# Optimization experiments

Measured on AMD Instinct MI355X. Metric: run time of the kernel, lower is better.

## Reference

```python
import jax, jax.numpy as jnp
import numpy as np
import math

B_SZ, T, D_IN, D_OUT, N = 8, 4096, 1024, 1024, 512
RMIN, RMAX, MAX_PHASE = 0.9, 1.0, 6.283


def setup_inputs() -> dict:
    key = jax.random.key(0)
    ks = jax.random.split(key, 9)
    x = jax.random.normal(ks[0], (B_SZ, T, D_IN), dtype=jnp.float32)
    u1 = jax.random.uniform(ks[1], (N,), dtype=jnp.float32)
    u2 = jax.random.uniform(ks[2], (N,), dtype=jnp.float32)
    nu_log = jnp.log(-0.5 * jnp.log(u1 * (RMAX + RMIN) * (RMAX - RMIN) + RMIN ** 2))
    theta_log = jnp.log(MAX_PHASE * u2)
    lam_mod = jnp.exp(-jnp.exp(nu_log))
    gamma_log = jnp.log(jnp.sqrt(1.0 - jnp.square(lam_mod)))
    B_re = jax.random.normal(ks[3], (N, D_IN), dtype=jnp.float32) / math.sqrt(2 * D_IN)
    B_im = jax.random.normal(ks[4], (N, D_IN), dtype=jnp.float32) / math.sqrt(2 * D_IN)
    C_re = jax.random.normal(ks[5], (D_OUT, N), dtype=jnp.float32) / math.sqrt(N)
    C_im = jax.random.normal(ks[6], (D_OUT, N), dtype=jnp.float32) / math.sqrt(N)
    D = jax.random.normal(ks[7], (D_OUT, D_IN), dtype=jnp.float32) / math.sqrt(D_IN)
    return {"x": x, "nu_log": nu_log, "theta_log": theta_log, "gamma_log": gamma_log,
            "B_re": B_re, "B_im": B_im, "C_re": C_re, "C_im": C_im, "D": D}


def reference(x, nu_log, theta_log, gamma_log, B_re, B_im, C_re, C_im, D):
    # Diagonal complex transition Lambda = exp(-exp(nu_log)) * exp(i*exp(theta_log))
    lam = jnp.exp(-jnp.exp(nu_log) + 1j * jnp.exp(theta_log))  # [N] complex64
    gamma = jnp.exp(gamma_log)  # [N]
    Bmat = B_re + 1j * B_im  # [N, D_IN]
    # Input projection for all timesteps at once: b_t = gamma * (B @ u_t)
    Bu = jnp.einsum('bti,ni->btn', x.astype(Bmat.dtype), Bmat) * gamma  # [B,T,N] complex
    # Parallel (associative) scan of x_t = lam * x_{t-1} + b_t over the time axis
    A = jnp.broadcast_to(lam, Bu.shape)

    def combine(e1, e2):
        a1, b1 = e1
        a2, b2 = e2
        return a1 * a2, a2 * b1 + b2

    _, states = jax.lax.associative_scan(combine, (A, Bu), axis=1)  # states: [B,T,N] complex
    Cmat = C_re + 1j * C_im  # [D_OUT, N]
    y = jnp.einsum('btn,on->bto', states, Cmat).real + jnp.einsum('bti,oi->bto', x, D)
    return y
```

## Files before the change

kernel.cpp:

```cpp
#include <hip/hip_runtime.h>
#include <stdint.h>


#define BSZ   8
#define TLEN  4096
#define DIN   1024
#define DOUT  1024
#define NST   512
#define M_TOT (BSZ * TLEN)
#define NC    32
#define CL    128

#define WOFF  8192
#define NBUF  16384

#define PLA   4096
#define OBUFS 12288

typedef __attribute__((ext_vector_type(8))) short bf16x8;
typedef __attribute__((ext_vector_type(4))) float f32x4;

__device__ __forceinline__ float s2f(short s) {
  unsigned v = ((unsigned)(unsigned short)s) << 16;
  return __builtin_bit_cast(float, v);
}
__device__ __forceinline__ short f2s_rne(float f) {
  unsigned u = __builtin_bit_cast(unsigned, f);
  unsigned r = (u + 0x7FFFu + ((u >> 16) & 1u)) >> 16;
  return (short)r;
}
__device__ __forceinline__ void round8(const float4 v0, const float4 v1, bf16x8& hv) {
  const float f[8] = {v0.x, v0.y, v0.z, v0.w, v1.x, v1.y, v1.z, v1.w};
  #pragma unroll
  for (int j = 0; j < 8; ++j) hv[j] = f2s_rne(f[j]);
}

__device__ __forceinline__ void gload16(const short* g, short* l) {
  __builtin_amdgcn_global_load_lds(
      (const __attribute__((address_space(1))) void*)g,
      (__attribute__((address_space(3))) void*)l, 16, 0, 0);
}


__device__ __forceinline__ void stage256(
    const short* __restrict__ Ag, const short* __restrict__ Wg,
    const int lda, const int ldb, const int m0, const int n0, const int k0,
    short* lbuf, const int w, const int lane)
{
  const int q  = (lane & 3) ^ ((lane >> 3) & 3);
  const int gr = lane >> 2;
  #pragma unroll
  for (int j = 0; j < 4; ++j) {
    const int ch = w * 4 + j;
    const short* g;
    int r0, ld, dst;
    if (ch < 16) { g = Ag; r0 = m0 + ch * 16;        ld = lda; dst = ch * 512; }
    else         { g = Wg; r0 = n0 + (ch - 16) * 16; ld = ldb; dst = WOFF + (ch - 16) * 512; }
    gload16(g + (size_t)(r0 + gr) * ld + k0 + q * 8, lbuf + dst);
  }
}

template<int NT>
__device__ __forceinline__ void gemm256(
    const short* __restrict__ Ap, const short* __restrict__ Wp,
    const int lda, const int ldb, const int m0, const int n0, const int tid,
    f32x4 (&acc)[8][4], short* lds)
{
  const int lane = tid & 63, w = tid >> 6, wm = w >> 2, wn = w & 3;
  const int lr = lane & 15, kg = lane >> 4;
  const int qo = (kg ^ ((lr >> 1) & 3)) * 8;

  stage256(Ap, Wp, lda, ldb, m0, n0, 0, lds, w, lane);

  for (int k = 0; k < NT; ++k) {
    short* cur = lds + (k & 1) * NBUF;
    if (k + 1 < NT) {
      stage256(Ap, Wp, lda, ldb, m0, n0, (k + 1) * 32,
               lds + ((k + 1) & 1) * NBUF, w, lane);
      asm volatile("s_waitcnt vmcnt(4)" ::: "memory");
    } else {
      asm volatile("s_waitcnt vmcnt(0)" ::: "memory");
    }
    __builtin_amdgcn_s_barrier();

    bf16x8 wv[4];
    #pragma unroll
    for (int ph = 0; ph < 2; ++ph) {
      if (ph == 0) {
        #pragma unroll
        for (int nf = 0; nf < 4; ++nf)
          wv[nf] = *(const bf16x8*)&cur[WOFF + (wn * 64 + nf * 16 + lr) * 32 + qo];
      }
      bf16x8 af[4];
      #pragma unroll
      for (int mi = 0; mi < 4; ++mi)
        af[mi] = *(const bf16x8*)&cur[(wm * 128 + (ph * 4 + mi) * 16 + lr) * 32 + qo];
      __builtin_amdgcn_s_barrier();
      asm volatile("s_waitcnt lgkmcnt(0)" ::: "memory");
      __builtin_amdgcn_sched_barrier(0);
      __builtin_amdgcn_s_setprio(1);
      #pragma unroll
      for (int nf = 0; nf < 4; ++nf)
        #pragma unroll
        for (int mi = 0; mi < 4; ++mi)
          acc[ph * 4 + mi][nf] =
              __builtin_amdgcn_mfma_f32_16x16x32_bf16(af[mi], wv[nf], acc[ph * 4 + mi][nf], 0, 0, 0);
      __builtin_amdgcn_s_setprio(0);
      __builtin_amdgcn_s_barrier();
    }
  }
}

__device__ __forceinline__ void map256(const int bid, int& mb, int& nb) {
  const int xcd = bid & 7;
  const int j   = bid >> 3;
  mb = xcd * 16 + (j >> 2);
  nb = j & 3;
}

__device__ __forceinline__ void stage_cx(
    const short* __restrict__ Ag, const short* __restrict__ Wg,
    const int lda, const int ldb, const int m0, const int n0, const int k0,
    short* lbuf, const int w, const int lane)
{
  const int q  = (lane & 3) ^ ((lane >> 3) & 3);
  const int gr = lane >> 2;
  #pragma unroll
  for (int j = 0; j < 3; ++j) {
    const int ch = w * 3 + j;
    const short* g;
    int r0, ld, dst;
    if (ch < 8) { g = Ag; r0 = m0 + ch * 16;        ld = lda; dst = ch * 512; }
    else        { g = Wg; r0 = n0 + (ch - 8) * 16;  ld = ldb; dst = PLA + (ch - 8) * 512; }
    gload16(g + (size_t)(r0 + gr) * ld + k0 + q * 8, lbuf + dst);
  }
}

__device__ __forceinline__ void gemm_fb(
    const float* __restrict__ Af, const short* __restrict__ Wp,
    const int lda, const int ldb, const int K, const int m0, const int n0, const int tid,
    f32x4 (&acc)[4][4], short* lds)
{
  const int lane = tid & 63, w = tid >> 6, wm = w >> 2, wn = w & 3;
  const int r = tid & 127, e = (tid >> 7) & 3;
  float4 pa[2];
  {
    const float* p = Af + (size_t)(m0 + r) * lda + e * 8;
    pa[0] = *(const float4*)(p);
    pa[1] = *(const float4*)(p + 4);
  }
  for (int k0 = 0; k0 < K; k0 += 32) {
    __syncthreads();
    {
      bf16x8 hv;
      round8(pa[0], pa[1], hv);
      const int f = (r >> 1) & 3;
      *(bf16x8*)&lds[r * 32 + ((e ^ f) * 8)] = hv;
    }
    {
      const int q = (lane & 3) ^ ((lane >> 3) & 3);
      const int gr = lane >> 2;
      #pragma unroll
      for (int i = 0; i < 2; ++i)
        gload16(Wp + (size_t)(n0 + (2 * w + i) * 16 + gr) * ldb + k0 + q * 8,
                lds + PLA + (2 * w + i) * 512);
    }
    __syncthreads();
    if (k0 + 32 < K) {
      const float* p = Af + (size_t)(m0 + r) * lda + (k0 + 32) + e * 8;
      pa[0] = *(const float4*)(p);
      pa[1] = *(const float4*)(p + 4);
    }
    const int lr = lane & 15, kg = lane >> 4;
    const int qo = (kg ^ ((lr >> 1) & 3)) * 8;
    bf16x8 aw[4], bw[4];
    #pragma unroll
    for (int mi = 0; mi < 4; ++mi)
      aw[mi] = *(const bf16x8*)&lds[(wm * 64 + mi * 16 + lr) * 32 + qo];
    #pragma unroll
    for (int ni = 0; ni < 4; ++ni)
      bw[ni] = *(const bf16x8*)&lds[PLA + (wn * 64 + ni * 16 + lr) * 32 + qo];
    #pragma unroll
    for (int ni = 0; ni < 4; ++ni)
      #pragma unroll
      for (int mi = 0; mi < 4; ++mi)
        acc[mi][ni] = __builtin_amdgcn_mfma_f32_16x16x32_bf16(aw[mi], bw[ni], acc[mi][ni], 0, 0, 0);
  }
  __syncthreads();
}

template<int NT>
__device__ __forceinline__ void gemm_pl(
    const short* __restrict__ Ap, const short* __restrict__ Wp,
    const int lda, const int ldb, const int m0, const int n0, const int tid,
    f32x4 (&acc)[4][4], short* lds)
{
  const int lane = tid & 63, w = tid >> 6, wm = w >> 2, wn = w & 3;
  const int lr = lane & 15, kg = lane >> 4;
  const int qo = (kg ^ ((lr >> 1) & 3)) * 8;
  stage_cx(Ap, Wp, lda, ldb, m0, n0, 0, lds, w, lane);
  for (int k = 0; k < NT; ++k) {
    short* cur = lds + (k & 1) * OBUFS;
    if (k + 1 < NT) {
      stage_cx(Ap, Wp, lda, ldb, m0, n0, (k + 1) * 32, lds + ((k + 1) & 1) * OBUFS, w, lane);
      asm volatile("s_waitcnt vmcnt(3)" ::: "memory");
    } else {
      asm volatile("s_waitcnt vmcnt(0)" ::: "memory");
    }
    __builtin_amdgcn_s_barrier();
    bf16x8 bw[4];
    #pragma unroll
    for (int ph = 0; ph < 2; ++ph) {
      if (ph == 0) {
        #pragma unroll
        for (int ni = 0; ni < 4; ++ni)
          bw[ni] = *(const bf16x8*)&cur[PLA + (wn * 64 + ni * 16 + lr) * 32 + qo];
      }
      const int mi0 = ph * 2;
      const bf16x8 a0 = *(const bf16x8*)&cur[(wm * 64 + mi0 * 16 + lr) * 32 + qo];
      const bf16x8 a1 = *(const bf16x8*)&cur[(wm * 64 + (mi0 + 1) * 16 + lr) * 32 + qo];
      __builtin_amdgcn_s_barrier();
      asm volatile("s_waitcnt lgkmcnt(0)" ::: "memory");
      __builtin_amdgcn_sched_barrier(0);
      __builtin_amdgcn_s_setprio(1);
      #pragma unroll
      for (int ni = 0; ni < 4; ++ni) {
        acc[mi0][ni]     = __builtin_amdgcn_mfma_f32_16x16x32_bf16(a0, bw[ni], acc[mi0][ni], 0, 0, 0);
        acc[mi0 + 1][ni] = __builtin_amdgcn_mfma_f32_16x16x32_bf16(a1, bw[ni], acc[mi0 + 1][ni], 0, 0, 0);
      }
      __builtin_amdgcn_s_setprio(0);
      __builtin_amdgcn_s_barrier();
    }
  }
}

__device__ __forceinline__ void map_mn4(const int bid, int& mb, int& nb) {
  const int xcd = bid & 7;
  const int j   = bid >> 3;
  mb = xcd * 32 + (j >> 2);
  nb = j & 3;
}

__global__ __launch_bounds__(256) void wround_k(const float* __restrict__ src,
    short* __restrict__ h, const int n4, const float sgn)
{
  const int i = blockIdx.x * 256 + threadIdx.x;
  if (i >= n4) return;
  const float4 v = ((const float4*)src)[i];
  short4 hv;
  hv.x = f2s_rne(sgn * v.x); hv.y = f2s_rne(sgn * v.y);
  hv.z = f2s_rne(sgn * v.z); hv.w = f2s_rne(sgn * v.w);
  ((short4*)h)[i] = hv;
}

__global__ __launch_bounds__(512, 2) void bu_mfma(
    const short* __restrict__ xw,
    const short* __restrict__ Brw, const short* __restrict__ Biw,
    const float* __restrict__ gamma,
    short* __restrict__ bu_re, short* __restrict__ bu_im)
{
  __shared__ short lds[2 * NBUF];
  f32x4 acc[8][4] = {};
  const int tid = threadIdx.x;
  int mb, nbk;
  map256(blockIdx.x, mb, nbk);
  const int m0  = mb * 256;
  const int n0s = nbk * 256;
  const bool re = (n0s < NST);
  const int nb0 = n0s & (NST - 1);

  gemm256<32>(xw, re ? Brw : Biw, DIN, DIN, m0, nb0, tid, acc, lds);

  short* Hp = re ? bu_re : bu_im;
  const int lane = tid & 63, w = tid >> 6, wm = w >> 2, wn = w & 3;
  const int lr = lane & 15, lq = lane >> 4;
  #pragma unroll
  for (int nf = 0; nf < 4; ++nf) {
    const int nb = nb0 + wn * 64 + nf * 16 + lr;
    const float g = gamma[nb];
    #pragma unroll
    for (int mf = 0; mf < 8; ++mf)
      #pragma unroll
      for (int j = 0; j < 4; ++j) {
        const size_t m = (size_t)m0 + wm * 128 + mf * 16 + lq * 4 + j;
        Hp[m * NST + nb] = f2s_rne(acc[mf][nf][j] * g);
      }
  }
}

__global__ __launch_bounds__(512, 4) void bu_fb(
    const float* __restrict__ x,
    const short* __restrict__ Brw, const short* __restrict__ Biw,
    const float* __restrict__ gamma,
    short* __restrict__ bu_re, short* __restrict__ bu_im)
{
  __shared__ short lds[2 * OBUFS];
  f32x4 acc[4][4] = {};
  const int tid = threadIdx.x;
  int mb, nbk;
  map_mn4(blockIdx.x, mb, nbk);
  const int m0  = mb * 128;
  const int n0s = nbk * 256;
  const bool re = (n0s < NST);
  const int nb0 = n0s & (NST - 1);
  gemm_fb(x, re ? Brw : Biw, DIN, DIN, DIN, m0, nb0, tid, acc, lds);
  short* Hp = re ? bu_re : bu_im;
  const int lane = tid & 63, w = tid >> 6, wm = w >> 2, wn = w & 3;
  const int lr = lane & 15, lq = lane >> 4;
  #pragma unroll
  for (int ni = 0; ni < 4; ++ni) {
    const int nb = nb0 + wn * 64 + ni * 16 + lr;
    const float g = gamma[nb];
    #pragma unroll
    for (int mi = 0; mi < 4; ++mi)
      #pragma unroll
      for (int j = 0; j < 4; ++j) {
        const size_t m = (size_t)m0 + wm * 64 + mi * 16 + lq * 4 + j;
        Hp[m * NST + nb] = f2s_rne(acc[mi][ni][j] * g);
      }
  }
}

__global__ void params_k(const float* __restrict__ nulog, const float* __restrict__ thlog,
                         const float* __restrict__ glog,
                         float2* __restrict__ lam, float2* __restrict__ lamL,
                         float* __restrict__ gamma)
{
  const int n = blockIdx.x * 256 + threadIdx.x;
  if (n >= NST) return;
  const float nu = expf(nulog[n]);
  const float th = expf(thlog[n]);
  const float mod = expf(-nu);
  float s, c;
  sincosf(th, &s, &c);
  lam[n] = make_float2(mod * c, mod * s);
  const float modL = expf(-(float)CL * nu);
  float sL, cL;
  sincosf((float)CL * th, &sL, &cL);
  lamL[n] = make_float2(modL * cL, modL * sL);
  gamma[n] = expf(glog[n]);
}

__global__ __launch_bounds__(256) void scan_partial(
    const short* __restrict__ bu_re, const short* __restrict__ bu_im,
    const float2* __restrict__ lam, float2* __restrict__ carry)
{
  const int g = blockIdx.x * 256 + threadIdx.x;
  const int n2 = g & 255;
  const int c  = (g >> 8) & (NC - 1);
  const int b  = g >> 13;
  const int n  = n2 * 2;
  const float2 L0 = lam[n], L1 = lam[n + 1];
  const short2* R = (const short2*)bu_re;
  const short2* I = (const short2*)bu_im;
  size_t idx = ((size_t)b * TLEN + (size_t)c * CL) * (NST / 2) + n2;
  float sr0 = 0.f, si0 = 0.f, sr1 = 0.f, si1 = 0.f;
  #pragma unroll 4
  for (int t = 0; t < CL; ++t, idx += NST / 2) {
    const short2 vr = R[idx], vi = I[idx];
    const float br0 = s2f(vr.x), br1 = s2f(vr.y);
    const float bi0 = s2f(vi.x), bi1 = s2f(vi.y);
    float nr = fmaf(L0.x, sr0, fmaf(-L0.y, si0, br0));
    float ni = fmaf(L0.x, si0, fmaf( L0.y, sr0, bi0));
    sr0 = nr; si0 = ni;
    nr = fmaf(L1.x, sr1, fmaf(-L1.y, si1, br1));
    ni = fmaf(L1.x, si1, fmaf( L1.y, sr1, bi1));
    sr1 = nr; si1 = ni;
  }
  const size_t cb = (size_t)(b * NC + c) * NST + n;
  carry[cb]     = make_float2(sr0, si0);
  carry[cb + 1] = make_float2(sr1, si1);
}

__global__ __launch_bounds__(256) void scan_carry(
    float2* __restrict__ carry, const float2* __restrict__ lamL)
{
  const int g = blockIdx.x * 256 + threadIdx.x;
  const int n = g & (NST - 1);
  const int b = g >> 9;
  const float2 P = lamL[n];
  float sr = 0.f, si = 0.f;
  for (int c = 0; c < NC; ++c) {
    const size_t idx = (size_t)(b * NC + c) * NST + n;
    const float2 v = carry[idx];
    carry[idx] = make_float2(sr, si);
    const float nr = fmaf(P.x, sr, fmaf(-P.y, si, v.x));
    const float ni = fmaf(P.x, si, fmaf( P.y, sr, v.y));
    sr = nr; si = ni;
  }
}

__global__ __launch_bounds__(256) void scan_final(
    short* __restrict__ bu_re, short* __restrict__ bu_im,
    const float2* __restrict__ lam, const float2* __restrict__ carry)
{
  const int g = blockIdx.x * 256 + threadIdx.x;
  const int n2 = g & 255;
  const int c  = (g >> 8) & (NC - 1);
  const int b  = g >> 13;
  const int n  = n2 * 2;
  const float2 L0 = lam[n], L1 = lam[n + 1];
  const size_t cb = (size_t)(b * NC + c) * NST + n;
  const float2 ci0 = carry[cb], ci1 = carry[cb + 1];
  short2* R = (short2*)bu_re;
  short2* I = (short2*)bu_im;
  size_t idx = ((size_t)b * TLEN + (size_t)c * CL) * (NST / 2) + n2;
  float sr0 = ci0.x, si0 = ci0.y, sr1 = ci1.x, si1 = ci1.y;
  #pragma unroll 4
  for (int t = 0; t < CL; ++t, idx += NST / 2) {
    const short2 vr = R[idx], vi = I[idx];
    const float br0 = s2f(vr.x), br1 = s2f(vr.y);
    const float bi0 = s2f(vi.x), bi1 = s2f(vi.y);
    float nr = fmaf(L0.x, sr0, fmaf(-L0.y, si0, br0));
    float ni = fmaf(L0.x, si0, fmaf( L0.y, sr0, bi0));
    sr0 = nr; si0 = ni;
    nr = fmaf(L1.x, sr1, fmaf(-L1.y, si1, br1));
    ni = fmaf(L1.x, si1, fmaf( L1.y, sr1, bi1));
    sr1 = nr; si1 = ni;
    short2 so;
    so.x = f2s_rne(sr0); so.y = f2s_rne(sr1);
    R[idx] = so;
    so.x = f2s_rne(si0); so.y = f2s_rne(si1);
    I[idx] = so;
  }
}

__global__ __launch_bounds__(512, 2) void out_mfma(
    const short* __restrict__ st_re, const short* __restrict__ st_im,
    const short* __restrict__ xw,
    const short* __restrict__ Crw, const short* __restrict__ Ciw,
    const short* __restrict__ Dw,
    float* __restrict__ y)
{
  __shared__ short lds[2 * NBUF];
  f32x4 acc[8][4] = {};
  const int tid = threadIdx.x;
  int mb, nbk;
  map256(blockIdx.x, mb, nbk);
  const int m0 = mb * 256;
  const int o0 = nbk * 256;

  gemm256<16>(st_re, Crw, NST, NST, m0, o0, tid, acc, lds);
  gemm256<16>(st_im, Ciw, NST, NST, m0, o0, tid, acc, lds);
  gemm256<32>(xw, Dw, DIN, DIN, m0, o0, tid, acc, lds);

  const int lane = tid & 63, w = tid >> 6, wm = w >> 2, wn = w & 3;
  const int lr = lane & 15, lq = lane >> 4;
  #pragma unroll
  for (int mf = 0; mf < 8; ++mf)
    #pragma unroll
    for (int j = 0; j < 4; ++j) {
      const size_t m = (size_t)m0 + wm * 128 + mf * 16 + lq * 4 + j;
      #pragma unroll
      for (int nf = 0; nf < 4; ++nf)
        y[m * DOUT + o0 + wn * 64 + nf * 16 + lr] = acc[mf][nf][j];
    }
}

__global__ __launch_bounds__(512, 4) void out_fb(
    const short* __restrict__ st_re, const short* __restrict__ st_im,
    const float* __restrict__ x,
    const short* __restrict__ Crw, const short* __restrict__ Ciw,
    const short* __restrict__ Dw,
    float* __restrict__ y)
{
  __shared__ short lds[2 * OBUFS];
  f32x4 acc[4][4] = {};
  const int tid = threadIdx.x;
  int mb, nbk;
  map_mn4(blockIdx.x, mb, nbk);
  const int m0 = mb * 128;
  const int o0 = nbk * 256;
  gemm_pl<16>(st_re, Crw, NST, NST, m0, o0, tid, acc, lds);
  gemm_pl<16>(st_im, Ciw, NST, NST, m0, o0, tid, acc, lds);
  gemm_fb(x, Dw, DIN, DIN, DIN, m0, o0, tid, acc, lds);
  const int lane = tid & 63, w = tid >> 6, wm = w >> 2, wn = w & 3;
  const int lr = lane & 15, lq = lane >> 4;
  #pragma unroll
  for (int mi = 0; mi < 4; ++mi)
    #pragma unroll
    for (int j = 0; j < 4; ++j) {
      const size_t m = (size_t)m0 + wm * 64 + mi * 16 + lq * 4 + j;
      #pragma unroll
      for (int ni = 0; ni < 4; ++ni)
        y[m * DOUT + o0 + wn * 64 + ni * 16 + lr] = acc[mi][ni][j];
    }
}

extern "C" void kernel_launch(void* const* d_in, const int* in_sizes, int n_in,
                              void* d_out, int out_size, void* d_ws, size_t ws_size,
                              hipStream_t stream)
{
  (void)in_sizes; (void)n_in; (void)out_size;
  const float* x     = (const float*)d_in[0];
  const float* nulog = (const float*)d_in[1];
  const float* thlog = (const float*)d_in[2];
  const float* glog  = (const float*)d_in[3];
  const float* Bre   = (const float*)d_in[4];
  const float* Bim   = (const float*)d_in[5];
  const float* Cre   = (const float*)d_in[6];
  const float* Cim   = (const float*)d_in[7];
  const float* Dm    = (const float*)d_in[8];
  float* y = (float*)d_out;

  const size_t PLANE  = (size_t)M_TOT * NST;
  const size_t XPLANE = (size_t)M_TOT * DIN;
  short*  bu_re = (short*)d_ws;
  short*  bu_im = bu_re + PLANE;
  float2* carry = (float2*)(bu_im + PLANE);
  float2* lam   = carry + (size_t)BSZ * NC * NST;
  float2* lamL  = lam + NST;
  float*  gamma = (float*)(lamL + NST);

  char* wp = (char*)(gamma + NST);
  wp = (char*)(((uintptr_t)wp + 255) & ~(uintptr_t)255);
  short* Brw = (short*)wp;
  short* Biw = Brw + (size_t)NST * DIN;
  short* Crw = Biw + (size_t)NST * DIN;
  short* Ciw = Crw + (size_t)DOUT * NST;
  short* Dw  = Ciw + (size_t)DOUT * NST;
  short* xw  = Dw  + (size_t)DOUT * DIN;
  const size_t needed_full = (size_t)((char*)(xw + XPLANE) - (char*)d_ws);
  const bool full = (ws_size >= needed_full);

  params_k<<<2, 256, 0, stream>>>(nulog, thlog, glog, lam, lamL, gamma);

  const int nB4 = (NST * DIN) / 4, nC4 = (DOUT * NST) / 4, nD4 = (DOUT * DIN) / 4;
  wround_k<<<(nB4 + 255) / 256, 256, 0, stream>>>(Bre, Brw, nB4,  1.0f);
  wround_k<<<(nB4 + 255) / 256, 256, 0, stream>>>(Bim, Biw, nB4,  1.0f);
  wround_k<<<(nC4 + 255) / 256, 256, 0, stream>>>(Cre, Crw, nC4,  1.0f);
  wround_k<<<(nC4 + 255) / 256, 256, 0, stream>>>(Cim, Ciw, nC4, -1.0f);
  wround_k<<<(nD4 + 255) / 256, 256, 0, stream>>>(Dm,  Dw,  nD4,  1.0f);

  if (full) {
    const int nX4 = (int)(XPLANE / 4);
    wround_k<<<(nX4 + 255) / 256, 256, 0, stream>>>(x, xw, nX4, 1.0f);
    bu_mfma<<<512, 512, 0, stream>>>(xw, Brw, Biw, gamma, bu_re, bu_im);
  } else {
    bu_fb<<<1024, 512, 0, stream>>>(x, Brw, Biw, gamma, bu_re, bu_im);
  }

  scan_partial<<<(BSZ * NC * (NST / 2)) / 256, 256, 0, stream>>>(bu_re, bu_im, lam, carry);
  scan_carry<<<(BSZ * NST) / 256, 256, 0, stream>>>(carry, lamL);
  scan_final<<<(BSZ * NC * (NST / 2)) / 256, 256, 0, stream>>>(bu_re, bu_im, lam, carry);

  if (full) {
    out_mfma<<<512, 512, 0, stream>>>(bu_re, bu_im, xw, Crw, Ciw, Dw, y);
  } else {
    out_fb<<<1024, 512, 0, stream>>>(bu_re, bu_im, x, Crw, Ciw, Dw, y);
  }
}
```

Measured before the change: 314.4 us.

## Triple-buffer GEMM LDS staging with prefetch distance two, spread across phases

The shared bf16 GEMM main loop moves from a double-buffered LDS ring with one-tile-ahead prefetch to a triple-buffered ring that prefetches two K-tiles ahead. The global→LDS loads for tile k+2 are split into one load per compute phase, and each K-step now runs four smaller MFMA phases instead of two. The aim is to hide more global memory latency and spread load issue across the MFMA work. In exchange, LDS per block grows from 64 KB to 96 KB, which may no longer fit two 512-thread blocks per CU. It also adds more barriers per K-step.

Result: faster. 307.5 us (-2.2%).

```diff
diff --git a/kernel.cpp b/kernel.cpp
--- a/kernel.cpp
+++ b/kernel.cpp
@@ -42,22 +42,18 @@
 }
 
 
-__device__ __forceinline__ void stage256(
+__device__ __forceinline__ void stage_one256(
     const short* __restrict__ Ag, const short* __restrict__ Wg,
     const int lda, const int ldb, const int m0, const int n0, const int k0,
-    short* lbuf, const int w, const int lane)
+    short* lbuf, const int ch, const int lane)
 {
   const int q  = (lane & 3) ^ ((lane >> 3) & 3);
   const int gr = lane >> 2;
-  #pragma unroll
-  for (int j = 0; j < 4; ++j) {
-    const int ch = w * 4 + j;
-    const short* g;
-    int r0, ld, dst;
-    if (ch < 16) { g = Ag; r0 = m0 + ch * 16;        ld = lda; dst = ch * 512; }
-    else         { g = Wg; r0 = n0 + (ch - 16) * 16; ld = ldb; dst = WOFF + (ch - 16) * 512; }
-    gload16(g + (size_t)(r0 + gr) * ld + k0 + q * 8, lbuf + dst);
-  }
+  const short* g;
+  int r0, ld, dst;
+  if (ch < 16) { g = Ag; r0 = m0 + ch * 16;        ld = lda; dst = ch * 512; }
+  else         { g = Wg; r0 = n0 + (ch - 16) * 16; ld = ldb; dst = WOFF + (ch - 16) * 512; }
+  gload16(g + (size_t)(r0 + gr) * ld + k0 + q * 8, lbuf + dst);
 }
 
 template<int NT>
@@ -70,44 +66,49 @@
   const int lr = lane & 15, kg = lane >> 4;
   const int qo = (kg ^ ((lr >> 1) & 3)) * 8;
 
-  stage256(Ap, Wp, lda, ldb, m0, n0, 0, lds, w, lane);
-
+  #pragma unroll
+  for (int j = 0; j < 4; ++j)
+    stage_one256(Ap, Wp, lda, ldb, m0, n0, 0, lds, w * 4 + j, lane);
+  #pragma unroll
+  for (int j = 0; j < 4; ++j)
+    stage_one256(Ap, Wp, lda, ldb, m0, n0, 32, lds + NBUF, w * 4 + j, lane);
+
+  int c0 = 0;
   for (int k = 0; k < NT; ++k) {
-    short* cur = lds + (k & 1) * NBUF;
-    if (k + 1 < NT) {
-      stage256(Ap, Wp, lda, ldb, m0, n0, (k + 1) * 32,
-               lds + ((k + 1) & 1) * NBUF, w, lane);
-      asm volatile("s_waitcnt vmcnt(4)" ::: "memory");
-    } else {
-      asm volatile("s_waitcnt vmcnt(0)" ::: "memory");
-    }
+    short* cur = lds + c0 * NBUF;
+    int cs = c0 + 2; if (cs >= 3) cs -= 3;
+    short* nx2 = lds + cs * NBUF;
+
+    if (k + 1 < NT) asm volatile("s_waitcnt vmcnt(4)" ::: "memory");
+    else            asm volatile("s_waitcnt vmcnt(0)" ::: "memory");
     __builtin_amdgcn_s_barrier();
 
     bf16x8 wv[4];
     #pragma unroll
-    for (int ph = 0; ph < 2; ++ph) {
+    for (int ph = 0; ph < 4; ++ph) {
       if (ph == 0) {
         #pragma unroll
         for (int nf = 0; nf < 4; ++nf)
           wv[nf] = *(const bf16x8*)&cur[WOFF + (wn * 64 + nf * 16 + lr) * 32 + qo];
       }
-      bf16x8 af[4];
-      #pragma unroll
-      for (int mi = 0; mi < 4; ++mi)
-        af[mi] = *(const bf16x8*)&cur[(wm * 128 + (ph * 4 + mi) * 16 + lr) * 32 + qo];
+      const int mi0 = ph * 2;
+      const bf16x8 a0 = *(const bf16x8*)&cur[(wm * 128 + mi0 * 16 + lr) * 32 + qo];
+      const bf16x8 a1 = *(const bf16x8*)&cur[(wm * 128 + (mi0 + 1) * 16 + lr) * 32 + qo];
+      if (k + 2 < NT)
+        stage_one256(Ap, Wp, lda, ldb, m0, n0, (k + 2) * 32, nx2, w * 4 + ph, lane);
       __builtin_amdgcn_s_barrier();
       asm volatile("s_waitcnt lgkmcnt(0)" ::: "memory");
       __builtin_amdgcn_sched_barrier(0);
       __builtin_amdgcn_s_setprio(1);
       #pragma unroll
-      for (int nf = 0; nf < 4; ++nf)
-        #pragma unroll
-        for (int mi = 0; mi < 4; ++mi)
-          acc[ph * 4 + mi][nf] =
-              __builtin_amdgcn_mfma_f32_16x16x32_bf16(af[mi], wv[nf], acc[ph * 4 + mi][nf], 0, 0, 0);
+      for (int nf = 0; nf < 4; ++nf) {
+        acc[mi0][nf]     = __builtin_amdgcn_mfma_f32_16x16x32_bf16(a0, wv[nf], acc[mi0][nf], 0, 0, 0);
+        acc[mi0 + 1][nf] = __builtin_amdgcn_mfma_f32_16x16x32_bf16(a1, wv[nf], acc[mi0 + 1][nf], 0, 0, 0);
+      }
       __builtin_amdgcn_s_setprio(0);
       __builtin_amdgcn_s_barrier();
     }
+    c0 = (c0 == 2) ? 0 : c0 + 1;
   }
 }
 
@@ -259,7 +260,7 @@
     const float* __restrict__ gamma,
     short* __restrict__ bu_re, short* __restrict__ bu_im)
 {
-  __shared__ short lds[2 * NBUF];
+  __shared__ short lds[3 * NBUF];
   f32x4 acc[8][4] = {};
   const int tid = threadIdx.x;
   int mb, nbk;
@@ -432,7 +433,7 @@
     const short* __restrict__ Dw,
     float* __restrict__ y)
 {
-  __shared__ short lds[2 * NBUF];
+  __shared__ short lds[3 * NBUF];
   f32x4 acc[8][4] = {};
   const int tid = threadIdx.x;
   int mb, nbk;
```
